# Optimization experiments

Hardware: AMD Instinct MI355X
Metric: run time of the kernel (lower is better)

Reference implementation:

```python
import jax, jax.numpy as jnp
from jax import lax
import numpy as np

U = 512          # LSTMOutUnits
NL = 3           # stacked LSTM cells
EMB = 300
VOCAB = 50000
LABELS = 7
BN_EPS = 1e-3    # keras BatchNormalization default epsilon


def _lstm_cell(x, h, c, W, Uw, b):
    # keras LSTMCell: gates ordered i, f, g(c), o; activation=softsign, recurrent_activation=sigmoid
    z = x @ W + h @ Uw + b                      # [B, 4U]
    i, f, g, o = jnp.split(z, 4, axis=-1)
    c = jax.nn.sigmoid(f) * c + jax.nn.sigmoid(i) * jax.nn.soft_sign(g)
    h = jax.nn.sigmoid(o) * jax.nn.soft_sign(c)
    return h, c


def _run_stack(x_tbd, Ws, Us, bs):
    # x_tbd: [T, B, D]; returns final hidden state of top cell: [B, U]
    B = x_tbd.shape[1]
    init = tuple((jnp.zeros((B, U), x_tbd.dtype), jnp.zeros((B, U), x_tbd.dtype)) for _ in range(NL))

    def step(carry, x):
        new = []
        inp = x
        for (h, c), W, Uw, b in zip(carry, Ws, Us, bs):
            h, c = _lstm_cell(inp, h, c, W, Uw, b)
            new.append((h, c))
            inp = h
        return tuple(new), None

    carry, _ = lax.scan(step, init, x_tbd)
    return carry[-1][0]


def setup_inputs() -> dict:
    key = jax.random.key(0)
    ks = iter(jax.random.split(key, 40))
    d = {}
    d['ids'] = jax.random.randint(next(ks), (128, 128), 0, VOCAB, dtype=jnp.int32)
    d['emb'] = jax.random.normal(next(ks), (VOCAB, EMB), jnp.float32)
    for pre in ('f', 'b'):
        for l in range(NL):
            din = EMB if l == 0 else U
            d[f'{pre}W{l}'] = jax.random.normal(next(ks), (din, 4 * U), jnp.float32) * 0.05
            d[f'{pre}U{l}'] = jax.random.normal(next(ks), (U, 4 * U), jnp.float32) * 0.05
            d[f'{pre}b{l}'] = jnp.zeros((4 * U,), jnp.float32)
    d['d0_W'] = jax.random.normal(next(ks), (U, U // 2), jnp.float32) * 0.05
    d['d0_b'] = jnp.zeros((U // 2,), jnp.float32)
    d['bn_gamma'] = jnp.ones((U // 2,), jnp.float32)
    d['bn_beta'] = jnp.zeros((U // 2,), jnp.float32)
    d['bn_mean'] = jnp.zeros((U // 2,), jnp.float32)
    d['bn_var'] = jnp.ones((U // 2,), jnp.float32)
    d['prelu_alpha'] = jnp.full((U // 2,), 0.25, jnp.float32)
    d['d1_W'] = jax.random.normal(next(ks), (U // 2, LABELS), jnp.float32) * 0.05
    d['d1_b'] = jnp.zeros((LABELS,), jnp.float32)
    return d


def reference(ids, emb,
              fW0, fU0, fb0, fW1, fU1, fb1, fW2, fU2, fb2,
              bW0, bU0, bb0, bW1, bU1, bb1, bW2, bU2, bb2,
              d0_W, d0_b, bn_gamma, bn_beta, bn_mean, bn_var,
              prelu_alpha, d1_W, d1_b):
    x = lax.stop_gradient(jnp.take(emb, ids, axis=0))      # [B, T, EMB]
    x = jnp.transpose(x, (1, 0, 2))                        # [T, B, EMB]
    fwd = _run_stack(x, (fW0, fW1, fW2), (fU0, fU1, fU2), (fb0, fb1, fb2))
    bwd = _run_stack(x[::-1], (bW0, bW1, bW2), (bU0, bU1, bU2), (bb0, bb1, bb2))
    add = 0.5 * (fwd + bwd)                                # [B, U]
    h = add @ d0_W + d0_b                                  # [B, U//2]
    h = (h - bn_mean) * lax.rsqrt(bn_var + BN_EPS) * bn_gamma + bn_beta
    h = jnp.where(h > 0, h, prelu_alpha * h)               # PReLU
    logits = h @ d1_W + d1_b                               # [B, LABELS]
    return jax.nn.softmax(logits, axis=-1)
```

## Files before the change

### kernel.cpp

```cpp
#include <hip/hip_runtime.h>
#include <hip/hip_bf16.h>
#include <math.h>

#define TT   128
#define BB   128
#define UU   512
#define EMBD 300
#define EMBP 320
#define NBLK 192
#define DBLK 96
#define NTHR 512
#define BSTR 1032

using bf16x8 = __attribute__((ext_vector_type(8))) short;
using f32x4  = __attribute__((ext_vector_type(4))) float;

#define NEED_WS 111681536ull
static void* g_pool = nullptr;
__attribute__((constructor)) static void alloc_pool() {
    if (hipMalloc(&g_pool, 120ull * 1024ull * 1024ull) != hipSuccess) g_pool = nullptr;
}

__device__ __forceinline__ float b2f(unsigned short u) {
    union { unsigned int i; float f; } v; v.i = ((unsigned int)u) << 16; return v.f;
}
__device__ __forceinline__ unsigned short f2b(float f) {
    union { unsigned int i; float f; } v; v.f = f;
    unsigned int i = v.i;
    return (unsigned short)((i + 0x7fffu + ((i >> 16) & 1u)) >> 16);
}
__device__ __forceinline__ unsigned short ld_bf(const void* p, size_t i, int f32) {
    return f32 ? f2b(((const float*)p)[i]) : ((const unsigned short*)p)[i];
}
__device__ __forceinline__ float ld_f(const void* p, size_t i, int f32) {
    return f32 ? ((const float*)p)[i] : b2f(((const unsigned short*)p)[i]);
}
__device__ __forceinline__ float clampz(float x) {
    return fminf(fmaxf(x, -60.0f), 60.0f);
}
__device__ __forceinline__ float sigm(float x)  { return 1.0f / (1.0f + __expf(-x)); }
__device__ __forceinline__ float ssign(float x) { return x / (1.0f + fabsf(x)); }

__device__ __forceinline__ int detect_f32(const void* emb) {
    const unsigned int* w = (const unsigned int*)emb;
    int cnt = 0;
    #pragma unroll
    for (int i = 0; i < 64; ++i) {
        unsigned int e = (w[i] >> 23) & 0xFFu;
        cnt += (e >= 96u && e <= 159u) ? 1 : 0;
    }
    return cnt >= 48;
}

struct P {
    const int* ids;
    const void* emb;
    const void* Wm[2][3];
    const void* Um[2][3];
    const void* bm[2][3];
    const void *d0W, *d0b;
    const void *bn_gamma, *bn_beta, *bn_mean, *bn_var;
    const void *alpha, *d1W, *d1b;
    unsigned short* X;
    unsigned short* H;
    float* hf;
    unsigned int* flags;
    unsigned int* epoch;
    float* out;
};

#define EPOFF 64

__device__ __forceinline__ unsigned int ald(const unsigned int* a) {
    return __hip_atomic_load(a, __ATOMIC_RELAXED, __HIP_MEMORY_SCOPE_AGENT);
}
__device__ __forceinline__ void ast(unsigned int* a, unsigned int v) {
    __hip_atomic_store(a, v, __ATOMIC_RELAXED, __HIP_MEMORY_SCOPE_AGENT);
}

__device__ __forceinline__ void gsync_fence(unsigned int* flags, unsigned int gen) {
    __syncthreads();
    if (threadIdx.x == 0) {
        __threadfence();
        ast(&flags[blockIdx.x], gen);
    }
    if (threadIdx.x < 64) {
        const int i = threadIdx.x;
        for (;;) {
            bool ok = true;
            #pragma unroll
            for (int j = 0; j < NBLK / 64; ++j)
                ok = ok && (ald(&flags[i + j * 64]) >= gen);
            if (__all(ok)) break;
            __builtin_amdgcn_s_sleep(1);
        }
        __threadfence();
    }
    __syncthreads();
}

__device__ __forceinline__ void gsync_dir(P& p, int dirbase, int eidx, int isagg, unsigned int gen) {
    __syncthreads();
    if (threadIdx.x == 0)
        ast(&p.flags[blockIdx.x], gen);
    if (isagg && threadIdx.x < 64) {
        const unsigned int* f = p.flags + dirbase + threadIdx.x;
        const bool two = (threadIdx.x < DBLK - 64);
        for (;;) {
            bool ok = (ald(f) >= gen) && (!two || (ald(f + 64) >= gen));
            if (__all(ok)) break;
            __builtin_amdgcn_s_sleep(1);
        }
        if (threadIdx.x == 0)
            ast(&p.epoch[eidx], gen);
    }
    if (threadIdx.x < 64) {
        const unsigned int* e = &p.epoch[eidx];
        while (ald(e) < gen) __builtin_amdgcn_s_sleep(1);
    }
    __syncthreads();
}

__device__ __forceinline__ void gsync_all(P& p, int dirbase, int eidx, int isagg, unsigned int gen) {
    __syncthreads();
    if (threadIdx.x == 0)
        ast(&p.flags[blockIdx.x], gen);
    if (isagg && threadIdx.x < 64) {
        const unsigned int* f = p.flags + dirbase + threadIdx.x;
        const bool two = (threadIdx.x < DBLK - 64);
        for (;;) {
            bool ok = (ald(f) >= gen) && (!two || (ald(f + 64) >= gen));
            if (__all(ok)) break;
            __builtin_amdgcn_s_sleep(1);
        }
        if (threadIdx.x == 0)
            ast(&p.epoch[eidx], gen);
    }
    if (threadIdx.x < 64) {
        while (!((ald(&p.epoch[0]) >= gen) && (ald(&p.epoch[EPOFF]) >= gen)))
            __builtin_amdgcn_s_sleep(1);
    }
    __syncthreads();
}

template<int K1T, int BOFF>
__device__ __forceinline__ void mfma_part(
    const unsigned short* __restrict__ a0p,
    const unsigned short* __restrict__ bp,
    f32x4 (&acc)[4])
{
    #pragma unroll 4
    for (int kt = 0; kt < K1T; kt += 32) {
        bf16x8 av = *(const bf16x8*)(a0p + kt);
        #pragma unroll
        for (int ct = 0; ct < 4; ++ct) {
            bf16x8 bv = *(const bf16x8*)(bp + (size_t)ct * 16 * BSTR + BOFF + kt);
            acc[ct] = __builtin_amdgcn_mfma_f32_16x16x32_bf16(av, bv, acc[ct], 0, 0, 0);
        }
    }
}

__global__ __launch_bounds__(NTHR, 1) void bilstm_persistent(P p) {
    const int blk = blockIdx.x;
    const int tid = threadIdx.x;

    const int f32 = detect_f32(p.emb);
    unsigned int gen = 0;

    __shared__ __align__(16) unsigned short Bt[64][BSTR];
    __shared__ __align__(16) float zbuf[8][2][16][17];
    __shared__ float hact[256];
    __shared__ float lgts[8];

    for (int row = blk; row < TT * BB; row += NBLK) {
        int t = row >> 7, b = row & 127;
        int id = p.ids[b * TT + t];
        unsigned short* xr = p.X + (size_t)row * EMBP;
        for (int k2 = tid; k2 < EMBP; k2 += NTHR)
            xr[k2] = (k2 < EMBD) ? ld_bf(p.emb, (size_t)id * EMBD + k2, f32)
                                 : (unsigned short)0;
    }
    gsync_fence(p.flags, ++gen);

    const int dir     = (blk >= DBLK) ? 1 : 0;
    const int rb      = blk - dir * DBLK;
    const int layer   = rb >> 5;
    const int dirbase = dir * DBLK;
    const int eidx    = dir * EPOFF;
    const int isagg   = (rb == 0);
    const int j0      = (rb & 31) * 16;

    const int wv   = tid >> 6;
    const int lane = tid & 63;
    const int l15  = lane & 15;
    const int quad = lane >> 4;

    const int row16 = lane & 15;
    const int jp    = (lane >> 4) & 1;
    const int ch    = lane >> 5;

    const int r0   = wv * 16 + l15;
    const int ko   = quad * 8;

    float cS[2][2];
    cS[0][0] = cS[0][1] = cS[1][0] = cS[1][1] = 0.0f;

    const size_t seq = (size_t)TT * BB * UU;

    const int KW   = (layer == 0) ? EMBD : UU;
    const int K1   = (layer == 0) ? EMBP : UU;
    const int Ktot = K1 + UU;
    const void* Wmat = p.Wm[dir][layer];
    const void* Umat = p.Um[dir][layer];
    const void* bias = p.bm[dir][layer];
    {
        int n = tid >> 3, ks = tid & 7;
        int wcol = ((n >> 2) & 3) * UU + j0 + (n >> 4) * 4 + (n & 3);
        for (int k2 = ks; k2 < Ktot; k2 += 8) {
            unsigned short v;
            if (k2 < KW)      v = ld_bf(Wmat, (size_t)k2 * 2048 + wcol, f32);
            else if (k2 < K1) v = 0;
            else              v = ld_bf(Umat, (size_t)(k2 - K1) * 2048 + wcol, f32);
            Bt[n][k2] = v;
        }
    }
    float bz[2][4][2];
    #pragma unroll
    for (int pp = 0; pp < 2; ++pp) {
        const int cb = j0 + (2 * pp + ch) * 4 + 2 * jp;
        #pragma unroll
        for (int g = 0; g < 4; ++g) {
            bz[pp][g][0] = ld_f(bias, g * UU + cb,     f32);
            bz[pp][g][1] = ld_f(bias, g * UU + cb + 1, f32);
        }
    }
    __syncthreads();

    unsigned short*       Hl  = p.H + (size_t)(layer * 2 + dir) * seq;
    const unsigned short* Hin = (layer > 0) ? (p.H + (size_t)((layer - 1) * 2 + dir) * seq) : nullptr;

    const unsigned short* bp = &Bt[l15][ko];
    float* zbw = &zbuf[wv][0][0][0];

    for (int s = 0; s < TT + 2; ++s) {
        const int t = s - layer;
        if (t >= 0 && t < TT) {
            const unsigned short* A2 = (t > 0) ? (Hl + (size_t)(t - 1) * BB * UU) : nullptr;

            f32x4 acc[4];
            #pragma unroll
            for (int ct = 0; ct < 4; ++ct) acc[ct] = f32x4{0.f, 0.f, 0.f, 0.f};

            if (layer == 0) {
                int tx = dir ? (TT - 1 - t) : t;
                const unsigned short* A1 = p.X + (size_t)tx * BB * EMBP;
                mfma_part<EMBP, 0>(A1 + (size_t)r0 * EMBP + ko, bp, acc);
                if (A2)
                    mfma_part<UU, EMBP>(A2 + (size_t)r0 * UU + ko, bp, acc);
            } else {
                const unsigned short* A1 = Hin + (size_t)t * BB * UU;
                mfma_part<UU, 0>(A1 + (size_t)r0 * UU + ko, bp, acc);
                if (A2)
                    mfma_part<UU, UU>(A2 + (size_t)r0 * UU + ko, bp, acc);
            }

            #pragma unroll
            for (int pp = 0; pp < 2; ++pp) {
                #pragma unroll
                for (int cth = 0; cth < 2; ++cth) {
                    const int ct = pp * 2 + cth;
                    #pragma unroll
                    for (int r = 0; r < 4; ++r)
                        zbw[cth * 272 + (quad * 4 + r) * 17 + l15] = acc[ct][r];
                }
                const int zb0 = ch * 272 + row16 * 17 + 2 * jp;
                float ziA = clampz(zbw[zb0 +  0] + bz[pp][0][0]);
                float zfA = clampz(zbw[zb0 +  4] + bz[pp][1][0]);
                float zgA = clampz(zbw[zb0 +  8] + bz[pp][2][0]);
                float zoA = clampz(zbw[zb0 + 12] + bz[pp][3][0]);
                float ziB = clampz(zbw[zb0 +  1] + bz[pp][0][1]);
                float zfB = clampz(zbw[zb0 +  5] + bz[pp][1][1]);
                float zgB = clampz(zbw[zb0 +  9] + bz[pp][2][1]);
                float zoB = clampz(zbw[zb0 + 13] + bz[pp][3][1]);
                float cpA = (t == 0) ? 0.0f : cS[pp][0];
                float cpB = (t == 0) ? 0.0f : cS[pp][1];
                float cnA = sigm(zfA) * cpA + sigm(ziA) * ssign(zgA);
                float cnB = sigm(zfB) * cpB + sigm(ziB) * ssign(zgB);
                cS[pp][0] = cnA; cS[pp][1] = cnB;
                float hA = sigm(zoA) * ssign(cnA);
                float hB = sigm(zoB) * ssign(cnB);
                const int R   = wv * 16 + row16;
                const int col = j0 + (2 * pp + ch) * 4 + 2 * jp;
                unsigned int pk = (unsigned int)f2b(hA) | ((unsigned int)f2b(hB) << 16);
                __hip_atomic_store((unsigned int*)&Hl[(size_t)t * BB * UU + (size_t)R * UU + col],
                                   pk, __ATOMIC_RELAXED, __HIP_MEMORY_SCOPE_AGENT);
                if (layer == 2 && t == TT - 1) {
                    size_t o = (size_t)dir * BB * UU + (size_t)R * UU + col;
                    __hip_atomic_store(&p.hf[o],     hA, __ATOMIC_RELAXED, __HIP_MEMORY_SCOPE_AGENT);
                    __hip_atomic_store(&p.hf[o + 1], hB, __ATOMIC_RELAXED, __HIP_MEMORY_SCOPE_AGENT);
                }
            }
        }
        gsync_dir(p, dirbase, eidx, isagg, ++gen);
    }

    gsync_all(p, dirbase, eidx, isagg, ++gen);

    if (blk < BB) {
        const int b = blk;
        if (tid < 256) {
            const float* h0 = p.hf + (size_t)b * UU;
            const float* h1 = p.hf + (size_t)BB * UU + (size_t)b * UU;
            float acc = ld_f(p.d0b, tid, f32);
            #pragma unroll 8
            for (int k = 0; k < UU; ++k) {
                float a = 0.5f * (h0[k] + h1[k]);
                acc = fmaf(a, ld_f(p.d0W, (size_t)k * 256 + tid, f32), acc);
            }
            acc = fminf(fmaxf(acc, -1e6f), 1e6f);
            float x = (acc - ld_f(p.bn_mean, tid, f32))
                      * rsqrtf(fmaxf(ld_f(p.bn_var, tid, f32), 0.0f) + 1e-3f)
                      * ld_f(p.bn_gamma, tid, f32) + ld_f(p.bn_beta, tid, f32);
            float al = ld_f(p.alpha, tid, f32);
            hact[tid] = (x > 0.f) ? x : al * x;
        }
        __syncthreads();
        if (tid < 7) {
            float s = ld_f(p.d1b, tid, f32);
            #pragma unroll 8
            for (int k = 0; k < 256; ++k)
                s = fmaf(hact[k], ld_f(p.d1W, k * 7 + tid, f32), s);
            lgts[tid] = fminf(fmaxf(s, -1e6f), 1e6f);
        }
        __syncthreads();
        if (tid == 0) {
            float mx = lgts[0];
            for (int j = 1; j < 7; ++j) mx = fmaxf(mx, lgts[j]);
            float ex[7]; float sum = 0.f;
            for (int j = 0; j < 7; ++j) { ex[j] = __expf(lgts[j] - mx); sum += ex[j]; }
            float inv = 1.0f / sum;
            for (int j = 0; j < 7; ++j) p.out[b * 7 + j] = ex[j] * inv;
        }
    }
}

extern "C" void kernel_launch(void* const* d_in, const int* in_sizes, int n_in,
                              void* d_out, int out_size, void* d_ws, size_t ws_size,
                              hipStream_t stream) {
    (void)in_sizes; (void)n_in; (void)out_size;

    P p;
    p.ids = (const int*)d_in[0];
    p.emb = d_in[1];
    for (int l = 0; l < 3; ++l) {
        p.Wm[0][l] = d_in[2 + l * 3];
        p.Um[0][l] = d_in[3 + l * 3];
        p.bm[0][l] = d_in[4 + l * 3];
        p.Wm[1][l] = d_in[11 + l * 3];
        p.Um[1][l] = d_in[12 + l * 3];
        p.bm[1][l] = d_in[13 + l * 3];
    }
    p.d0W      = d_in[20];
    p.d0b      = d_in[21];
    p.bn_gamma = d_in[22];
    p.bn_beta  = d_in[23];
    p.bn_mean  = d_in[24];
    p.bn_var   = d_in[25];
    p.alpha    = d_in[26];
    p.d1W      = d_in[27];
    p.d1b      = d_in[28];

    char* base = (ws_size >= NEED_WS || g_pool == nullptr) ? (char*)d_ws : (char*)g_pool;
    const size_t OFF_X  = 8192;
    const size_t OFF_H  = OFF_X + (size_t)TT * BB * EMBP * 2;
    const size_t OFF_HF = OFF_H + (size_t)3 * 2 * TT * BB * UU * 2;
    p.flags = (unsigned int*)base;
    p.epoch = (unsigned int*)(base + 4096);
    p.X     = (unsigned short*)(base + OFF_X);
    p.H     = (unsigned short*)(base + OFF_H);
    p.hf    = (float*)(base + OFF_HF);
    p.out   = (float*)d_out;

    hipMemsetAsync(base, 0, 8192, stream);
    hipLaunchKernelGGL(bilstm_persistent, dim3(NBLK), dim3(NTHR), 0, stream, p);
}
```

Before: 1.674 ms.

## Replace aggregator-epoch grid barrier with direct all-wave flag polling; pad LDS stride

The per-step barrier no longer goes through an aggregator block that publishes an epoch word. Every wave of every block now polls the flag array of its direction directly, which removes one hop of global-memory latency per timestep. The final barrier polls all 192 flags directly as well. The shared-memory stride BSTR also changes from 1032 to 1056, which alters the bank mapping of weight reads. The trade-offs are much more polling traffic on the flags, and the trailing __syncthreads is dropped in gsync_dir, so the waves in a block now leave the barrier on their own.

```diff
diff --git a/kernel.cpp b/kernel.cpp
--- a/kernel.cpp
+++ b/kernel.cpp
@@ -10,7 +10,7 @@
 #define NBLK 192
 #define DBLK 96
 #define NTHR 512
-#define BSTR 1032
+#define BSTR 1056
 
 using bf16x8 = __attribute__((ext_vector_type(8))) short;
 using f32x4  = __attribute__((ext_vector_type(4))) float;
@@ -69,8 +69,6 @@
     float* out;
 };
 
-#define EPOFF 64
-
 __device__ __forceinline__ unsigned int ald(const unsigned int* a) {
     return __hip_atomic_load(a, __ATOMIC_RELAXED, __HIP_MEMORY_SCOPE_AGENT);
 }
@@ -99,46 +97,31 @@
     __syncthreads();
 }
 
-__device__ __forceinline__ void gsync_dir(P& p, int dirbase, int eidx, int isagg, unsigned int gen) {
+__device__ __forceinline__ void gsync_dir(P& p, int dirbase, unsigned int gen) {
     __syncthreads();
     if (threadIdx.x == 0)
         ast(&p.flags[blockIdx.x], gen);
-    if (isagg && threadIdx.x < 64) {
-        const unsigned int* f = p.flags + dirbase + threadIdx.x;
-        const bool two = (threadIdx.x < DBLK - 64);
-        for (;;) {
-            bool ok = (ald(f) >= gen) && (!two || (ald(f + 64) >= gen));
-            if (__all(ok)) break;
-            __builtin_amdgcn_s_sleep(1);
-        }
-        if (threadIdx.x == 0)
-            ast(&p.epoch[eidx], gen);
-    }
-    if (threadIdx.x < 64) {
-        const unsigned int* e = &p.epoch[eidx];
-        while (ald(e) < gen) __builtin_amdgcn_s_sleep(1);
-    }
-    __syncthreads();
-}
-
-__device__ __forceinline__ void gsync_all(P& p, int dirbase, int eidx, int isagg, unsigned int gen) {
+    const int lane = threadIdx.x & 63;
+    const unsigned int* f = p.flags + dirbase + lane;
+    const bool two = lane < (DBLK - 64);
+    for (;;) {
+        bool ok = (ald(f) >= gen) && (!two || (ald(f + 64) >= gen));
+        if (__all(ok)) break;
+        __builtin_amdgcn_s_sleep(1);
+    }
+}
+
+__device__ __forceinline__ void gsync_all(P& p, unsigned int gen) {
     __syncthreads();
     if (threadIdx.x == 0)
         ast(&p.flags[blockIdx.x], gen);
-    if (isagg && threadIdx.x < 64) {
-        const unsigned int* f = p.flags + dirbase + threadIdx.x;
-        const bool two = (threadIdx.x < DBLK - 64);
-        for (;;) {
-            bool ok = (ald(f) >= gen) && (!two || (ald(f + 64) >= gen));
-            if (__all(ok)) break;
-            __builtin_amdgcn_s_sleep(1);
-        }
-        if (threadIdx.x == 0)
-            ast(&p.epoch[eidx], gen);
-    }
-    if (threadIdx.x < 64) {
-        while (!((ald(&p.epoch[0]) >= gen) && (ald(&p.epoch[EPOFF]) >= gen)))
-            __builtin_amdgcn_s_sleep(1);
+    const int lane = threadIdx.x & 63;
+    for (;;) {
+        bool ok = (ald(&p.flags[lane]) >= gen) &&
+                  (ald(&p.flags[lane + 64]) >= gen) &&
+                  (ald(&p.flags[lane + 128]) >= gen);
+        if (__all(ok)) break;
+        __builtin_amdgcn_s_sleep(1);
     }
     __syncthreads();
 }
@@ -186,8 +169,6 @@
     const int rb      = blk - dir * DBLK;
     const int layer   = rb >> 5;
     const int dirbase = dir * DBLK;
-    const int eidx    = dir * EPOFF;
-    const int isagg   = (rb == 0);
     const int j0      = (rb & 31) * 16;
 
     const int wv   = tid >> 6;
@@ -301,10 +282,10 @@
                 }
             }
         }
-        gsync_dir(p, dirbase, eidx, isagg, ++gen);
-    }
-
-    gsync_all(p, dirbase, eidx, isagg, ++gen);
+        gsync_dir(p, dirbase, ++gen);
+    }
+
+    gsync_all(p, ++gen);
 
     if (blk < BB) {
         const int b = blk;
```

New measurement: 1.992 ms. 19.0% more time.
